# Performance work log

Hardware: AMD Instinct MI355X
Metric: run time of the kernel (lower is better)

Reference implementation:

```python
import jax, jax.numpy as jnp
import numpy as np
from jax.scipy.special import logsumexp

# static problem sizes (all graphs identical size; pairs interleaved [q0,c0,q1,c1,...])
B = 64; NG = 2 * B; N = 48; E = 192; MAX_N = 64; MAX_E = 256
D_IN = 32; D = 128; EDGE_EMB = 128; M = 256; S = 64
T = 5; K = 3; TEMP = 0.1; SINK_ITERS = 10
VN = NG * N; VE = NG * E


def _mlp2(x, W1, b1, W2, b2):
    return jnp.maximum(x @ W1 + b1, 0.0) @ W2 + b2


def setup_inputs():
    keys = iter(jax.random.split(jax.random.key(0), 64))
    def w(fan_in, fan_out):
        return jax.random.normal(next(keys), (fan_in, fan_out), dtype=jnp.float32) * (1.0 / float(np.sqrt(fan_in)))
    z = lambda n: jnp.zeros((n,), jnp.float32)
    inp = {}
    inp['node_features'] = jax.random.normal(next(keys), (VN, D_IN), dtype=jnp.float32)
    inp['edge_features'] = jax.random.normal(next(keys), (VE, D_IN), dtype=jnp.float32)
    off = jnp.repeat(jnp.arange(NG, dtype=jnp.int32) * N, E)
    inp['from_idx'] = jax.random.randint(next(keys), (VE,), 0, N, dtype=jnp.int32) + off
    inp['to_idx'] = jax.random.randint(next(keys), (VE,), 0, N, dtype=jnp.int32) + off
    inp['enc_node_W'] = w(D_IN, D); inp['enc_node_b'] = z(D)
    inp['enc_edge_W'] = w(D_IN, EDGE_EMB); inp['enc_edge_b'] = z(EDGE_EMB)
    inp['ni_W1'] = w(2 * D, 2 * D); inp['ni_b1'] = z(2 * D)
    inp['ni_W2'] = w(2 * D, D); inp['ni_b2'] = z(D)
    ei_in = M + EDGE_EMB
    inp['ei_W1'] = w(ei_in, ei_in); inp['ei_b1'] = z(ei_in)
    inp['ei_W2'] = w(ei_in, EDGE_EMB); inp['ei_b2'] = z(EDGE_EMB)
    inp['msg_W'] = w(2 * D + EDGE_EMB, M); inp['msg_b'] = z(M)
    inp['nu_W1'] = w(D + M, 2 * D); inp['nu_b1'] = z(2 * D)
    inp['nu_W2'] = w(2 * D, D); inp['nu_b2'] = z(D)
    inp['ns_W1'] = w(D, S); inp['ns_b1'] = z(S)
    inp['ns_W2'] = w(S, S); inp['ns_b2'] = z(S)
    inp['es_W1'] = w(M, S); inp['es_b1'] = z(S)
    inp['es_W2'] = w(S, S); inp['es_b2'] = z(S)
    return inp


def _forward(node_features, edge_features, enc_node_W, enc_node_b, enc_edge_W, enc_edge_b,
             ni_W1, ni_b1, ni_W2, ni_b2, ei_W1, ei_b1, ei_W2, ei_b2, msg_W, msg_b,
             nu_W1, nu_b1, nu_W2, nu_b2, ns_W1, ns_b1, ns_W2, ns_b2,
             es_W1, es_b1, es_W2, es_b2, from_idx, to_idx):
    enc_n = node_features @ enc_node_W + enc_node_b            # [VN, D]
    enc_e = edge_features @ enc_edge_W + enc_edge_b            # [VE, EDGE_EMB]
    node_store = jnp.zeros((VN, D * (T + 1)), jnp.float32)
    edge_store = jnp.zeros((VE, M * (T + 1)), jnp.float32)
    # flat index of node/edge j of graph g inside interleaved padded store: g*max + j
    node_pad_idx = (jnp.arange(NG)[:, None] * MAX_N + jnp.arange(N)[None, :]).reshape(-1)
    edge_pad_idx = (jnp.arange(NG)[:, None] * MAX_E + jnp.arange(E)[None, :]).reshape(-1)
    node_mask = (jnp.arange(MAX_N) < N).astype(jnp.float32)[None, :, None]
    edge_mask = (jnp.arange(MAX_E) < E).astype(jnp.float32)[None, :, None]

    def transport(store, n_per, max_set, fdim, sW1, sb1, sW2, sb2, mask):
        x = store.reshape(NG, n_per, store.shape[-1])
        x = jnp.pad(x, ((0, 0), (0, max_set - n_per), (0, 0)))   # pad to max set size
        q, c = x[0::2], x[1::2]                                   # [B, max, dim_total]
        fq, fc = q[:, :, -fdim:], c[:, :, -fdim:]
        tq = _mlp2(fq, sW1, sb1, sW2, sb2) * mask
        tc = _mlp2(fc, sW1, sb1, sW2, sb2) * mask
        la = jnp.einsum('bqs,bcs->bqc', tq, tc) / TEMP
        for _ in range(SINK_ITERS):
            la = la - logsumexp(la, axis=2, keepdims=True)
            la = la - logsumexp(la, axis=1, keepdims=True)
        plan = jnp.exp(la)
        qi = jnp.einsum('bqc,bcd->bqd', plan, c)                  # query <- corpus
        ci = jnp.einsum('bqc,bqd->bcd', plan, q)                  # corpus <- query
        inter = jnp.stack([qi, ci], axis=1).reshape(NG * max_set, -1)
        return plan, inter, fq, fc

    for _ in range(K):  # time_update_steps
        h, e = enc_n, enc_e
        node_slots = [jnp.zeros((VN, D), jnp.float32)]
        edge_slots = [jnp.zeros((VE, M), jnp.float32)]
        for p in range(1, T + 1):  # propagation_steps
            h_comb = _mlp2(jnp.concatenate([h, node_store[:, (p - 1) * D:p * D]], -1), ni_W1, ni_b1, ni_W2, ni_b2)
            e_comb = _mlp2(jnp.concatenate([e, edge_store[:, (p - 1) * M:p * M]], -1), ei_W1, ei_b1, ei_W2, ei_b2)
            src, dst = h_comb[from_idx], h_comb[to_idx]
            fwd_msg = jnp.concatenate([src, dst, e_comb], -1) @ msg_W + msg_b
            bwd_msg = jnp.concatenate([dst, src, e_comb], -1) @ msg_W + msg_b
            agg = jax.ops.segment_sum(fwd_msg, to_idx, num_segments=VN) + jax.ops.segment_sum(bwd_msg, from_idx, num_segments=VN)
            h = _mlp2(jnp.concatenate([h_comb, agg], -1), nu_W1, nu_b1, nu_W2, nu_b2)
            src2, dst2 = h[from_idx], h[to_idx]
            msgs = (jnp.concatenate([src2, dst2, e_comb], -1) @ msg_W + msg_b) + \
                   (jnp.concatenate([dst2, src2, e_comb], -1) @ msg_W + msg_b)
            node_slots.append(h)
            edge_slots.append(msgs)
        upd_node = jnp.concatenate(node_slots, axis=1)
        upd_edge = jnp.concatenate(edge_slots, axis=1)
        n_plan, n_inter, ffq, ffc = transport(upd_node, N, MAX_N, D, ns_W1, ns_b1, ns_W2, ns_b2, node_mask)
        _, e_inter, _, _ = transport(upd_edge, E, MAX_E, M, es_W1, es_b1, es_W2, es_b2, edge_mask)
        node_store = jnp.concatenate([jnp.zeros((VN, D), jnp.float32), n_inter[node_pad_idx, D:]], axis=1)
        edge_store = jnp.concatenate([jnp.zeros((VE, M), jnp.float32), e_inter[edge_pad_idx, M:]], axis=1)

    # feature_alignment_score: -sum relu(q - P c)
    score = -jnp.sum(jnp.maximum(ffq - jnp.einsum('bqc,bcd->bqd', n_plan, ffc), 0.0), axis=(1, 2))
    return score


def reference(node_features, edge_features, from_idx, to_idx, enc_node_W, enc_node_b, enc_edge_W, enc_edge_b,
              ni_W1, ni_b1, ni_W2, ni_b2, ei_W1, ei_b1, ei_W2, ei_b2, msg_W, msg_b,
              nu_W1, nu_b1, nu_W2, nu_b2, ns_W1, ns_b1, ns_W2, ns_b2,
              es_W1, es_b1, es_W2, es_b2):
    return _forward(node_features, edge_features, enc_node_W, enc_node_b, enc_edge_W, enc_edge_b,
                    ni_W1, ni_b1, ni_W2, ni_b2, ei_W1, ei_b1, ei_W2, ei_b2, msg_W, msg_b,
                    nu_W1, nu_b1, nu_W2, nu_b2, ns_W1, ns_b1, ns_W2, ns_b2,
                    es_W1, es_b1, es_W2, es_b2, from_idx, to_idx)
```

## Files before the change

### kernel.cpp

```cpp
#include <hip/hip_runtime.h>
#include <cstdint>
#include <cstddef>

#define NGg   128
#define Bb    64
#define Nn    48
#define Ee    192
#define Sdim  64
#define VNn   6144
#define VEe   24576
#define INV_TEMP 10.0f
#define ADJ_STRIDE 96

typedef unsigned short u16;
typedef unsigned int   u32;
typedef __attribute__((ext_vector_type(8))) short short8;
typedef __attribute__((ext_vector_type(4))) float floatx4;

__device__ __forceinline__ u16 f2bf(float f)
{
    unsigned int u = __float_as_uint(f);
    u += 0x7FFFu + ((u >> 16) & 1u);
    return (u16)(u >> 16);
}
__device__ __forceinline__ float bf2f(u16 h)
{
    return __uint_as_float(((unsigned int)h) << 16);
}

__device__ __forceinline__ u32 packhl(float v)
{
    u16 h = f2bf(v);
    u16 l = f2bf(v - bf2f(h));
    return (u32)h | ((u32)l << 16);
}
__device__ __forceinline__ float unpackhl(u32 w)
{
    return __uint_as_float(w << 16) + __uint_as_float(w & 0xFFFF0000u);
}

#define FL_RELU  1
#define FL_OUTPK 4

#define TW 40

template<int BM, int BN>
__global__ __launch_bounds__(256) void gemm_pk_kernel(
    const u32* __restrict__ A1, int lda1, int K1,
    const u32* __restrict__ A2, int lda2, int K2,
    const u16* __restrict__ Wh, const u16* __restrict__ Wl, int ldwt,
    const float* __restrict__ bias,
    void* __restrict__ Cv, int ldc,
    int Ncap, int flags)
{
    constexpr int FM = BM / 32;
    constexpr int FN = BN / 32;
    constexpr int NA = BM / 8;
    constexpr int NB = BN / 8;
    __shared__ __align__(16) u16 Ah[BM * TW];
    __shared__ __align__(16) u16 Al[BM * TW];
    __shared__ __align__(16) u16 Bh[BN * TW];
    __shared__ __align__(16) u16 Bl[BN * TW];
    const int tid = threadIdx.x;
    const int lane = tid & 63, wave = tid >> 6;
    const int wm = wave >> 1, wn = wave & 1;
// ... 98 lines not shown
                          const u32* A2, int lda2, int K2,
                          const u16* Wh, const u16* Wl, int ldwt,
                          const float* bias,
                          void* C, int ldc, int M, int Ngrid, int Ncap, int flags)
{
    dim3 grid(Ngrid / BN, M / BM);
    if (BM == 128 && BN == 128)
        gemm_pk_kernel<128, 128><<<grid, 256, 0, s>>>(A1, lda1, K1, A2, lda2, K2, Wh, Wl, ldwt, bias, C, ldc, Ncap, flags);
    else if (BM == 128 && BN == 64)
        gemm_pk_kernel<128, 64><<<grid, 256, 0, s>>>(A1, lda1, K1, A2, lda2, K2, Wh, Wl, ldwt, bias, C, ldc, Ncap, flags);
    else if (BM == 64 && BN == 128)
        gemm_pk_kernel<64, 128><<<grid, 256, 0, s>>>(A1, lda1, K1, A2, lda2, K2, Wh, Wl, ldwt, bias, C, ldc, Ncap, flags);
    else
        gemm_pk_kernel<64, 64><<<grid, 256, 0, s>>>(A1, lda1, K1, A2, lda2, K2, Wh, Wl, ldwt, bias, C, ldc, Ncap, flags);
}

struct GemmDesc {
    const u32* A1; int lda1, K1;
    const u32* A2; int lda2, K2;
    const u16* Wh; const u16* Wl; int ldwt;
    const float* bias;
    void* C; int ldc;
    int Ncap, flags, nx, nblk;
};

static inline GemmDesc mkDesc(const u32* A1, int lda1, int K1,
                              const u32* A2, int lda2, int K2,
                              const u16* Wh, const u16* Wl, int ldwt,
                              const float* bias, void* C, int ldc,
                              int M, int Ngrid, int Ncap, int flags)
{
    GemmDesc d;
    d.A1 = A1; d.lda1 = lda1; d.K1 = K1;
    d.A2 = A2; d.lda2 = lda2; d.K2 = K2;
    d.Wh = Wh; d.Wl = Wl; d.ldwt = ldwt;
    d.bias = bias; d.C = C; d.ldc = ldc;
    d.Ncap = Ncap; d.flags = flags;
    d.nx = Ngrid / 128; d.nblk = (M / 128) * (Ngrid / 128);
    return d;
}

__global__ __launch_bounds__(256) void gemm2_pk_kernel(GemmDesc d0, GemmDesc d1, int nb0)
{
    GemmDesc d;
    int local;
    if ((int)blockIdx.x < nb0) { d = d0; local = blockIdx.x; }
    else                       { d = d1; local = blockIdx.x - nb0; }
    const int by = local / d.nx, bx = local % d.nx;
    __shared__ __align__(16) u16 Ah[128 * TW];
    __shared__ __align__(16) u16 Al[128 * TW];
    __shared__ __align__(16) u16 Bh[128 * TW];
    __shared__ __align__(16) u16 Bl[128 * TW];
    const int tid = threadIdx.x;
    const int lane = tid & 63, wave = tid >> 6;
    const int wm = wave >> 1, wn = wave & 1;
    const int bm = by * 128, bn = bx * 128;
    const int K = d.K1 + d.K2;
    const int srow = tid >> 1;
    const int skoff = (tid & 1) * 16;
    const int arow = bm + srow;
    const int brow = bn + srow;
// ... 39 lines not shown
        short8 afh[4], afl[4], bfh[4], bfl[4];
        #pragma unroll
        for (int i = 0; i < 4; i++) {
            const int ro = (wm * 64 + i * 16 + l15) * TW + lq * 8;
            afh[i] = *(const short8*)&Ah[ro];
            afl[i] = *(const short8*)&Al[ro];
        }
        #pragma unroll
        for (int j = 0; j < 4; j++) {
            const int ro = (wn * 64 + j * 16 + l15) * TW + lq * 8;
            bfh[j] = *(const short8*)&Bh[ro];
            bfl[j] = *(const short8*)&Bl[ro];
        }
        #pragma unroll
        for (int i = 0; i < 4; i++)
            #pragma unroll
            for (int j = 0; j < 4; j++) {
                acc[i][j] = __builtin_amdgcn_mfma_f32_16x16x32_bf16(afh[i], bfl[j], acc[i][j], 0, 0, 0);
                acc[i][j] = __builtin_amdgcn_mfma_f32_16x16x32_bf16(afl[i], bfh[j], acc[i][j], 0, 0, 0);
                acc[i][j] = __builtin_amdgcn_mfma_f32_16x16x32_bf16(afh[i], bfh[j], acc[i][j], 0, 0, 0);
            }
        __syncthreads();
    }
    const int relu = d.flags & FL_RELU;
    const int opk  = d.flags & FL_OUTPK;
    #pragma unroll
    for (int j = 0; j < 4; j++) {
        const int col = bn + wn * 64 + j * 16 + l15;
        const bool cok = (col < d.Ncap);
        const float bv = (d.bias && cok) ? d.bias[col] : 0.f;
        #pragma unroll
        for (int i = 0; i < 4; i++) {
            const int row0 = bm + wm * 64 + i * 16 + lq * 4;
            #pragma unroll
            for (int r = 0; r < 4; r++) {
                float v = acc[i][j][r] + bv;
                if (relu) v = fmaxf(v, 0.f);
                if (cok) {
                    if (opk)
                        ((u32*)d.C)[(size_t)(row0 + r) * d.ldc + col] = packhl(v);
                    else
                        ((float*)d.C)[(size_t)(row0 + r) * d.ldc + col] = v;
                }
            }
        }
    }
}

static inline void gemm2(hipStream_t s, const GemmDesc& d0, const GemmDesc& d1)
{
    gemm2_pk_kernel<<<d0.nblk + d1.nblk, 256, 0, s>>>(d0, d1, d0.nblk);
}

__global__ __launch_bounds__(256) void gemm_f32_kernel(
    const float* __restrict__ A, int lda, int K,
    const u16* __restrict__ Wh, const u16* __restrict__ Wl, int ldwt,
    const float* __restrict__ bias, u32* __restrict__ C, int ldc, int Ncap)
{
    __shared__ __align__(16) u16 Ah[128 * TW];
    __shared__ __align__(16) u16 Al[128 * TW];
    __shared__ __align__(16) u16 Bh[128 * TW];
    __shared__ __align__(16) u16 Bl[128 * TW];
    const int tid = threadIdx.x;
    const int lane = tid & 63, wave = tid >> 6;
    const int wm = wave >> 1, wn = wave & 1;
    const int bm = blockIdx.y * 128, bn = blockIdx.x * 128;
    const int srow = tid >> 1;
    const int skoff = (tid & 1) * 16;
    const int arow = bm + srow, brow = bn + srow;
    const int l15 = lane & 15, lq = lane >> 4;

    floatx4 acc[4][4];
    #pragma unroll
    for (int i = 0; i < 4; i++)
// ... 41 lines not shown
        }
        #pragma unroll
        for (int i = 0; i < 4; i++)
            #pragma unroll
            for (int j = 0; j < 4; j++) {
                acc[i][j] = __builtin_amdgcn_mfma_f32_16x16x32_bf16(afh[i], bfl[j], acc[i][j], 0, 0, 0);
                acc[i][j] = __builtin_amdgcn_mfma_f32_16x16x32_bf16(afl[i], bfh[j], acc[i][j], 0, 0, 0);
                acc[i][j] = __builtin_amdgcn_mfma_f32_16x16x32_bf16(afh[i], bfh[j], acc[i][j], 0, 0, 0);
            }
        __syncthreads();
    }
    #pragma unroll
    for (int j = 0; j < 4; j++) {
        const int col = bn + wn * 64 + j * 16 + l15;
        const bool cok = (col < Ncap);
        const float bv = cok ? bias[col] : 0.f;
        #pragma unroll
        for (int i = 0; i < 4; i++) {
            const int row0 = bm + wm * 64 + i * 16 + lq * 4;
            #pragma unroll
            for (int r = 0; r < 4; r++) {
                if (cok)
                    C[(size_t)(row0 + r) * ldc + col] = packhl(acc[i][j][r] + bv);
            }
        }
    }
}

__global__ __launch_bounds__(256) void gemm_ec2msgs_kernel(
    const u32* __restrict__ A,
    const u16* __restrict__ Wh, const u16* __restrict__ Wl, int ldwt,
    const float* __restrict__ bias,
    const float* __restrict__ Qs,
    const int* __restrict__ from_idx, const int* __restrict__ to_idx,
    u32* __restrict__ M)
{
    __shared__ __align__(16) u16 Ah[128 * TW];
    __shared__ __align__(16) u16 Al[128 * TW];
    __shared__ __align__(16) u16 Bh[128 * TW];
    __shared__ __align__(16) u16 Bl[128 * TW];
    const int tid = threadIdx.x;
    const int lane = tid & 63, wave = tid >> 6;
    const int wm = wave >> 1, wn = wave & 1;
    const int bm = blockIdx.y * 128, bn = blockIdx.x * 128;
    const int srow = tid >> 1;
    const int skoff = (tid & 1) * 16;

    floatx4 acc[4][4];
    #pragma unroll
    for (int i = 0; i < 4; i++)
        #pragma unroll
        for (int j = 0; j < 4; j++) acc[i][j] = (floatx4){0.f, 0.f, 0.f, 0.f};

    const int arow = bm + srow;
    const int brow = bn + srow;
    const int l15 = lane & 15, lq = lane >> 4;

    for (int k0 = 0; k0 < 128; k0 += 32) {
        const int kk = k0 + skoff;
        const u32* asrc = A + (size_t)arow * 128 + kk;
        u32 pk[16];
        ((uint4*)pk)[0] = ((const uint4*)asrc)[0];
        ((uint4*)pk)[1] = ((const uint4*)asrc)[1];
        ((uint4*)pk)[2] = ((const uint4*)asrc)[2];
        ((uint4*)pk)[3] = ((const uint4*)asrc)[3];
        u32 hi8[8], lo8[8];
        #pragma unroll
        for (int q = 0; q < 8; q++) {
            hi8[q] = __builtin_amdgcn_perm(pk[2 * q + 1], pk[2 * q], 0x05040100u);
            lo8[q] = __builtin_amdgcn_perm(pk[2 * q + 1], pk[2 * q], 0x07060302u);
        }
        *(uint4*)&Ah[srow * TW + skoff]     = ((uint4*)hi8)[0];
        *(uint4*)&Ah[srow * TW + skoff + 8] = ((uint4*)hi8)[1];
        *(uint4*)&Al[srow * TW + skoff]     = ((uint4*)lo8)[0];
        *(uint4*)&Al[srow * TW + skoff + 8] = ((uint4*)lo8)[1];
        const u16* bh = Wh + (size_t)brow * ldwt + kk;
        const u16* bl = Wl + (size_t)brow * ldwt + kk;
        *(uint4*)&Bh[srow * TW + skoff]     = ((const uint4*)bh)[0];
        *(uint4*)&Bh[srow * TW + skoff + 8] = ((const uint4*)bh)[1];
        *(uint4*)&Bl[srow * TW + skoff]     = ((const uint4*)bl)[0];
        *(uint4*)&Bl[srow * TW + skoff + 8] = ((const uint4*)bl)[1];
        __syncthreads();
        short8 afh[4], afl[4], bfh[4], bfl[4];
        #pragma unroll
        for (int i = 0; i < 4; i++) {
            const int ro = (wm * 64 + i * 16 + l15) * TW + lq * 8;
            afh[i] = *(const short8*)&Ah[ro];
            afl[i] = *(const short8*)&Al[ro];
        }
        #pragma unroll
        for (int j = 0; j < 4; j++) {
            const int ro = (wn * 64 + j * 16 + l15) * TW + lq * 8;
            bfh[j] = *(const short8*)&Bh[ro];
            bfl[j] = *(const short8*)&Bl[ro];
        }
        #pragma unroll
        for (int i = 0; i < 4; i++)
            #pragma unroll
            for (int j = 0; j < 4; j++) {
                acc[i][j] = __builtin_amdgcn_mfma_f32_16x16x32_bf16(afh[i], bfl[j], acc[i][j], 0, 0, 0);
                acc[i][j] = __builtin_amdgcn_mfma_f32_16x16x32_bf16(afl[i], bfh[j], acc[i][j], 0, 0, 0);
                acc[i][j] = __builtin_amdgcn_mfma_f32_16x16x32_bf16(afh[i], bfh[j], acc[i][j], 0, 0, 0);
            }
        __syncthreads();
    }
    #pragma unroll
    for (int i = 0; i < 4; i++) {
        #pragma unroll
        for (int r = 0; r < 4; r++) {
            const int row = bm + wm * 64 + i * 16 + lq * 4 + r;
            const int fi = from_idx[row], ti = to_idx[row];
            #pragma unroll
            for (int j = 0; j < 4; j++) {
                const int col = bn + wn * 64 + j * 16 + l15;
                float v = 2.f * (acc[i][j][r] + bias[col])
                        + Qs[(size_t)fi * 256 + col] + Qs[(size_t)ti * 256 + col];
                M[(size_t)row * 256 + col] = packhl(v);
            }
        }
    }
}

__global__ __launch_bounds__(256) void prep_kernel(
    const float* __restrict__ niW1, const float* __restrict__ niW2,
    const float* __restrict__ eiW1, const float* __restrict__ eiW2,
    const float* __restrict__ msgW, const float* __restrict__ nuW1,
    const float* __restrict__ nuW2, const float* __restrict__ encnW,
    const float* __restrict__ enceW, const float* __restrict__ nsW1,
    const float* __restrict__ nsW2, const float* __restrict__ esW1,
    const float* __restrict__ esW2,
    u16* __restrict__ WT, u16* __restrict__ WTL)
{
    int idx = blockIdx.x * 256 + threadIdx.x;
    if (idx >= 696320) return;
    const float* src; int base, N, Npad, ldk, noff = 0, wtoff;
    int wsum = 0;
    if      (idx < 65536)  { src = niW1;  base = 0;      N = 256; Npad = 256; ldk = 256; wtoff = 0; }
    else if (idx < 98304)  { src = niW2;  base = 65536;  N = 128; Npad = 128; ldk = 256; wtoff = 65536; }
    else if (idx < 245760) { src = eiW1;  base = 98304;  N = 384; Npad = 384; ldk = 384; wtoff = 98304; }
    else if (idx < 294912) { src = eiW2;  base = 245760; N = 128; Npad = 128; ldk = 384; wtoff = 245760; }
// ... 3 lines not shown
    else if (idx < 557056) { src = nuW1;  base = 458752; N = 256; Npad = 256; ldk = 384; wtoff = 458752; }
    else if (idx < 589824) { src = nuW2;  base = 557056; N = 128; Npad = 128; ldk = 256; wtoff = 557056; }
    else if (idx < 622592) { src = msgW;  base = 589824; N = 256; Npad = 256; ldk = 128; wtoff = 589824; wsum = 1; }
    else if (idx < 626688) { src = encnW; base = 622592; N = 128; Npad = 128; ldk = 32;  wtoff = 622592; }
    else if (idx < 630784) { src = enceW; base = 626688; N = 128; Npad = 128; ldk = 32;  wtoff = 626688; }
    else if (idx < 647168) { src = nsW1;  base = 630784; N = 64;  Npad = 128; ldk = 128; wtoff = 630784; }
    else if (idx < 655360) { src = nsW2;  base = 647168; N = 64;  Npad = 128; ldk = 64;  wtoff = 647168; }
    else if (idx < 688128) { src = esW1;  base = 655360; N = 64;  Npad = 128; ldk = 256; wtoff = 655360; }
    else                   { src = esW2;  base = 688128; N = 64;  Npad = 128; ldk = 64;  wtoff = 688128; }
    int rel = idx - base;
    int k = rel / Npad, n = rel % Npad;
    float v = 0.f;
    if (n < N) {
        v = src[(size_t)k * N + n];
        if (wsum) v += src[32768 + (size_t)k * N + n];
    }
    u16 h = f2bf(v);
    size_t o = (size_t)wtoff + (size_t)(noff + n) * ldk + k;
    WT[o] = h;
    WTL[o] = f2bf(v - bf2f(h));
}

__global__ __launch_bounds__(256) void bgemm_dual_kernel(
    const float* __restrict__ P, int ms, int n_per,
    const u32* __restrict__ U, int ldu,
    u32* __restrict__ C, int ldc, int nxh)
{
    __shared__ __align__(16) u16 Ah[64 * TW];
    __shared__ __align__(16) u16 Al[64 * TW];
    __shared__ __align__(16) u16 Bh[128 * TW];
    __shared__ __align__(16) u16 Bl[128 * TW];
    const int b = blockIdx.z;
    const float* Pb = P + (size_t)b * ms * ms;
    const int bxr = blockIdx.x;
    const int transp = (bxr >= nxh) ? 1 : 0;
    const int bn = (bxr - transp * nxh) * 128;
    const int qbase = (2 * b) * n_per, cbase = (2 * b + 1) * n_per;
    const int obase = transp ? cbase : qbase;
    const int ibase = transp ? qbase : cbase;
    const int bm = blockIdx.y * 64;
    const int tid = threadIdx.x, lane = tid & 63, wave = tid >> 6;
    const int wm = wave >> 1, wn = wave & 1;
    const int l15 = lane & 15, lq = lane >> 4;
    const int sar = tid >> 2, sak = (tid & 3) * 8;
    const int sbn = tid >> 1, sbk = (tid & 1) * 16;
    const int Kpad = (n_per + 31) & ~31;

    floatx4 acc[2][4];
    #pragma unroll
    for (int i = 0; i < 2; i++)
        #pragma unroll
        for (int j = 0; j < 4; j++) acc[i][j] = (floatx4){0.f, 0.f, 0.f, 0.f};

    for (int k0 = 0; k0 < Kpad; k0 += 32) {
        {
            u16 ph[8], pl8[8];
            const int m = bm + sar;
            #pragma unroll
            for (int i = 0; i < 8; i++) {
                int kk = k0 + sak + i;
                float v = 0.f;
                if (kk < n_per && m < n_per)
                    v = transp ? Pb[(size_t)kk * ms + m] : Pb[(size_t)m * ms + kk];
                u16 h = f2bf(v);
                ph[i] = h; pl8[i] = f2bf(v - bf2f(h));
            }
            *(uint4*)&Ah[sar * TW + sak] = *(const uint4*)&ph[0];
            *(uint4*)&Al[sar * TW + sak] = *(const uint4*)&pl8[0];
        }
        {
            u16 qh[16], ql[16];
            #pragma unroll
            for (int i = 0; i < 16; i++) {
                int kk = k0 + sbk + i;
                u32 w = 0;
                if (kk < n_per) w = U[(size_t)(ibase + kk) * ldu + bn + sbn];
                qh[i] = (u16)w; ql[i] = (u16)(w >> 16);
            }
            *(uint4*)&Bh[sbn * TW + sbk]     = *(const uint4*)&qh[0];
            *(uint4*)&Bh[sbn * TW + sbk + 8] = *(const uint4*)&qh[8];
            *(uint4*)&Bl[sbn * TW + sbk]     = *(const uint4*)&ql[0];
            *(uint4*)&Bl[sbn * TW + sbk + 8] = *(const uint4*)&ql[8];
        }
        __syncthreads();
        short8 afh[2], afl[2], bfh[4], bfl[4];
        #pragma unroll
        for (int i = 0; i < 2; i++) {
            const int ro = (wm * 32 + i * 16 + l15) * TW + lq * 8;
            afh[i] = *(const short8*)&Ah[ro];
            afl[i] = *(const short8*)&Al[ro];
        }
// ... 9 lines not shown
            for (int j = 0; j < 4; j++) {
                acc[i][j] = __builtin_amdgcn_mfma_f32_16x16x32_bf16(afh[i], bfl[j], acc[i][j], 0, 0, 0);
                acc[i][j] = __builtin_amdgcn_mfma_f32_16x16x32_bf16(afl[i], bfh[j], acc[i][j], 0, 0, 0);
                acc[i][j] = __builtin_amdgcn_mfma_f32_16x16x32_bf16(afh[i], bfh[j], acc[i][j], 0, 0, 0);
            }
        __syncthreads();
    }
    #pragma unroll
    for (int j = 0; j < 4; j++) {
        const int col = bn + wn * 64 + j * 16 + l15;
        #pragma unroll
        for (int i = 0; i < 2; i++) {
            const int row0 = bm + wm * 32 + i * 16 + lq * 4;
            #pragma unroll
            for (int r = 0; r < 4; r++) {
                const int m = row0 + r;
                if (m < n_per)
                    C[(size_t)(obase + m) * ldc + col] = packhl(acc[i][j][r]);
            }
        }
    }
}

static inline void bgemmDual(hipStream_t s, const float* P, int ms, int n_per,
                             const u32* U, int ldu, u32* C, int ldc, int N)
{
    int nxh = N / 128;
    dim3 grid(nxh * 2, (n_per + 63) / 64, Bb);
    bgemm_dual_kernel<<<grid, 256, 0, s>>>(P, ms, n_per, U, ldu, C, ldc, nxh);
}

__global__ __launch_bounds__(256) void la_sinkhorn64_kernel(
    const float* __restrict__ tt, float* __restrict__ n_la)
{
    const int b = blockIdx.x;
    __shared__ float Aq[64][65];
    __shared__ float Ac[64][65];
    __shared__ float m[64][65];
    __shared__ float v_s[64];
    __shared__ float part[4][64];
    const int tid = threadIdx.x;
    const int lane = tid & 63, w = tid >> 6;
    for (int idx = tid; idx < 4096; idx += 256) {
        int r = idx >> 6, s = idx & 63;
        float vq = 0.f, vc = 0.f;
        if (r < Nn) {
            vq = tt[((size_t)(2 * b) * Nn + r) * Sdim + s];
            vc = tt[((size_t)(2 * b + 1) * Nn + r) * Sdim + s];
        }
        Aq[r][s] = vq;
        Ac[r][s] = vc;
    }
    __syncthreads();
    {
        const int tx = tid & 15, ty = tid >> 4;
        float acc[4][4] = {};
// ... 28 lines not shown
        u[j] = mx;
    }
    for (int it = 0; it < 10; it++) {
        float vr = v_s[lane];
        #pragma unroll
        for (int j = 0; j < 16; j++) {
            float s = __expf(x[j] - vr - u[j]);
            #pragma unroll
            for (int d = 1; d < 64; d <<= 1) s += __shfl_xor(s, d);
            u[j] += __logf(s);
        }
        float s = 0.f;
        #pragma unroll
        for (int j = 0; j < 16; j++) s += __expf(x[j] - u[j] - vr);
        part[w][lane] = s;
        __syncthreads();
        if (tid < 64) {
            float ss = part[0][tid] + part[1][tid] + part[2][tid] + part[3][tid];
            v_s[tid] += __logf(ss);
        }
        __syncthreads();
    }
    float vr = v_s[lane];
    float* g = n_la + (size_t)b * 4096;
    #pragma unroll
    for (int j = 0; j < 16; j++)
        g[(size_t)(w * 16 + j) * 64 + lane] = __expf(x[j] - u[j] - vr);
}

__global__ __launch_bounds__(256) void la_gemm256_kernel(
    const float* __restrict__ tt, float* __restrict__ la)
{
    const int b = blockIdx.z;
    const int bm = blockIdx.y * 64, bn = blockIdx.x * 64;
    __shared__ float Aq[64][65];
    __shared__ float Ac[64][65];
    const int tid = threadIdx.x;
    for (int idx = tid; idx < 4096; idx += 256) {
        int r = idx >> 6, s = idx & 63;
        float vq = 0.f, vc = 0.f;
        int qr = bm + r, cr = bn + r;
        if (qr < Ee) vq = tt[((size_t)(2 * b) * Ee + qr) * Sdim + s];
        if (cr < Ee) vc = tt[((size_t)(2 * b + 1) * Ee + cr) * Sdim + s];
        Aq[r][s] = vq;
        Ac[r][s] = vc;
    }
    __syncthreads();
    const int tx = tid & 15, ty = tid >> 4;
    float acc[4][4] = {};
    for (int s = 0; s < 64; s++) {
// ... 50 lines not shown
            #pragma unroll
            for (int d = 1; d < 64; d <<= 1) s += __shfl_xor(s, d);
            u[j] += __logf(s);
            const float inv = 1.f / s;
            cp0 = fmaf(e0, inv, cp0);
            cp1 = fmaf(e1, inv, cp1);
            cp2 = fmaf(e2, inv, cp2);
            cp3 = fmaf(e3, inv, cp3);
        }
        *(float4*)&part[w][lane][0] = (float4){cp0, cp1, cp2, cp3};
        __syncthreads();
        if (tid < 256) {
            const int cl = tid >> 2, cq = tid & 3;
            float ss = 0.f;
            #pragma unroll
            for (int w2 = 0; w2 < 16; w2++) ss += part[w2][cl][cq];
            v_s[tid] += __logf(ss);
        }
        __syncthreads();
    }
    const float4 vr = *(const float4*)&v_s[4 * lane];
    #pragma unroll
    for (int j = 0; j < 16; j++) {
        float4 o;
        o.x = __expf(x[j].x - u[j] - vr.x);
        o.y = __expf(x[j].y - u[j] - vr.y);
        o.z = __expf(x[j].z - u[j] - vr.z);
        o.w = __expf(x[j].w - u[j] - vr.w);
        ((float4*)(g + (size_t)(w * 16 + j) * 256))[lane] = o;
    }
}

__global__ __launch_bounds__(256) void zero_deg_kernel(int* __restrict__ deg)
{
    deg[blockIdx.x * 256 + threadIdx.x] = 0;
}

__global__ __launch_bounds__(256) void csr_build_kernel(
    const int* __restrict__ from_idx, const int* __restrict__ to_idx,
    int* __restrict__ deg, u32* __restrict__ adj)
{
    int e = blockIdx.x * 256 + threadIdx.x;
    if (e >= VEe) return;
    int f = from_idx[e], t = to_idx[e];
    int p1 = atomicAdd(&deg[t], 1);
    if (p1 < ADJ_STRIDE) adj[(size_t)t * ADJ_STRIDE + p1] = ((u32)e << 13) | (u32)f;
    int p2 = atomicAdd(&deg[f], 1);
    if (p2 < ADJ_STRIDE) adj[(size_t)f * ADJ_STRIDE + p2] = ((u32)e << 13) | (u32)t;
}

__global__ __launch_bounds__(256) void agg_csr_kernel(
    const u32* __restrict__ P01,
// ... 16 lines not shown
        a += unpackhl(ec2[(size_t)e * 256 + d]) + unpackhl(P01[(size_t)pr * 512 + d]);
    }
    agg[(size_t)n * 256 + d] = packhl(a);
}

__global__ __launch_bounds__(256) void msgs_inplace_kernel(
    u32* __restrict__ m, const float* __restrict__ Qs,
    const int* __restrict__ from_idx, const int* __restrict__ to_idx)
{
    const int e = blockIdx.x;
    const int d = threadIdx.x;
    const int f = from_idx[e], t = to_idx[e];
    size_t o = (size_t)e * 256 + d;
    float v = Qs[(size_t)f * 256 + d] + Qs[(size_t)t * 256 + d] + 2.f * unpackhl(m[o]);
    m[o] = packhl(v);
}

__global__ void diag_kernel(float* __restrict__ out, float v)
{
    out[threadIdx.x] = v;
}

__global__ __launch_bounds__(128) void score_kernel(
    const u32* __restrict__ upd_node, const float* __restrict__ plan,
    float* __restrict__ out)
{
    const int b = blockIdx.x;
    const int tid = threadIdx.x;
    __shared__ float ffc[48][128];
    __shared__ float pl[64][48];
    __shared__ float red[128];
    for (int c = 0; c < 48; c++)
        ffc[c][tid] = unpackhl(upd_node[(size_t)((2 * b + 1) * 48 + c) * 640 + 512 + tid]);
    for (int idx = tid; idx < 64 * 48; idx += 128) {
        int q = idx / 48, c = idx % 48;
        pl[q][c] = plan[(size_t)b * 4096 + q * 64 + c];
    }
    __syncthreads();
    float accv = 0.f;
    for (int q = 0; q < 64; q++) {
        float rsum = 0.f;
        #pragma unroll 8
        for (int c = 0; c < 48; c++) rsum = fmaf(pl[q][c], ffc[c][tid], rsum);
        float fq = 0.f;
        if (q < 48) fq = unpackhl(upd_node[(size_t)((2 * b) * 48 + q) * 640 + 512 + tid]);
        accv += fmaxf(fq - rsum, 0.f);
    }
    red[tid] = accv;
    __syncthreads();
    for (int sft = 64; sft > 0; sft >>= 1) {
        if (tid < sft) red[tid] += red[tid + sft];
        __syncthreads();
    }
    if (tid == 0) out[b] = -red[0];
}

#define OFF_UPD_NODE   0ULL
#define OFF_NODE_STORE 3932160ULL
#define OFF_EDGE_STORE 7077888ULL
// ... 68 lines not shown
    const float* es_b2 = (const float*)d_in[29];

    float* ws = (float*)d_ws;
    float* upd_node   = ws + OFF_UPD_NODE;
    float* node_store = ws + OFF_NODE_STORE;
    float* edge_store = ws + OFF_EDGE_STORE;
    float* ecomb      = ws + OFF_ECOMB;
    float* enc_n      = ws + OFF_ENC_N;
    float* enc_e      = ws + OFF_ENC_E;
    float* n_la       = ws + OFF_N_LA;
    u16* WT  = (u16*)(ws + OFF_WT);
    u16* WTL = (u16*)(ws + OFF_WTL);
    float* arena      = ws + OFF_ARENA;
    int* deg = (int*)(ws + OFF_DEG);
    u32* adj = (u32*)(ws + OFF_ADJ);

    float* A_hidden = arena;
    float* A_hcomb  = arena + 1572864;
    float* A_ehid   = arena + 2359296;
    float* A_ec2    = arena + 2359296;
    float* A_P01    = arena + 8650752;
    float* A_aggb   = arena + 11796480;
    float* B_Qs       = arena;
    float* B_thid_e   = arena + 8650752;
    float* B_ttreal_e = arena + 10223616;
    float* B_ela      = arena + 2359296;
    float* B_msgs     = arena + 6553600;
    float* B_thid_n   = arena + 12058624;
    float* B_ttreal_n = arena + 12451840;

    prep_kernel<<<(696320 + 255) / 256, 256, 0, stream>>>(
        ni_W1, ni_W2, ei_W1, ei_W2, msg_W, nu_W1, nu_W2,
        enc_node_W, enc_edge_W, ns_W1, ns_W2, es_W1, es_W2, WT, WTL);
    zero_deg_kernel<<<VNn / 256, 256, 0, stream>>>(deg);
    csr_build_kernel<<<VEe / 256, 256, 0, stream>>>(from_idx, to_idx, deg, adj);

    gemm_f32_kernel<<<dim3(1, VNn / 128), 256, 0, stream>>>(
        node_features, 32, 32, WT + WT_ENCN, WTL + WT_ENCN, 32, enc_node_b, PK(enc_n), 128, 128);
    gemm_f32_kernel<<<dim3(1, VEe / 128), 256, 0, stream>>>(
        edge_features, 32, 32, WT + WT_ENCE, WTL + WT_ENCE, 32, enc_edge_b, PK(enc_e), 128, 128);

    for (int k = 0; k < 3; k++) {
        for (int p = 1; p <= 5; p++) {
            const bool hs = (k > 0) && (p > 1);
            const u32* hA1 = (p == 1) ? PK(enc_n) : PK(upd_node + (size_t)(p - 2) * 128);
            const int  hlda1 = (p == 1) ? 128 : 640;
// ... 36 lines not shown
                       ni_b2, A_hcomb, 128, VNn, 128, 128, FL_OUTPK);
                gemmPK(stream, 64, 128, PK(A_hcomb), 128, 128, nullptr, 0, 0,
                       WT + WT_P01, WTL + WT_P01, 128,
                       nullptr, A_P01, 512, VNn, 512, 512, FL_OUTPK);
            } else {
                gemmPK(stream, 64, 128, hA1, hlda1, 128, hA2, 512, hK2,
                       WT + WT_NIW1, WTL + WT_NIW1, 256, ni_b1,
                       A_hidden, 256, VNn, 256, 256, FL_RELU | FL_OUTPK);
                gemmPK(stream, 64, 64, PK(A_hidden), 256, 256, nullptr, 0, 0,
                       WT + WT_NIW2, WTL + WT_NIW2, 256,
                       ni_b2, A_hcomb, 128, VNn, 128, 128, FL_OUTPK);
                gemmPK(stream, 64, 128, PK(A_hcomb), 128, 128, nullptr, 0, 0,
                       WT + WT_P01, WTL + WT_P01, 128,
                       nullptr, A_P01, 512, VNn, 512, 512, FL_OUTPK);
            }
            agg_csr_kernel<<<VNn, 256, 0, stream>>>(PK(A_P01), PK(A_ec2), deg, adj, PK(A_aggb));
            gemmPK(stream, 64, 128, PK(A_hcomb), 128, 128, PK(A_aggb), 256, 256,
                   WT + WT_NUW1, WTL + WT_NUW1, 384,
                   nu_b1, A_hidden, 256, VNn, 256, 256, FL_RELU | FL_OUTPK);
            gemmPK(stream, 64, 64, PK(A_hidden), 256, 256, nullptr, 0, 0,
                   WT + WT_NUW2, WTL + WT_NUW2, 256,
                   nu_b2, upd_node + (size_t)(p - 1) * 128, 640, VNn, 128, 128, FL_OUTPK);
        }
        gemmPK(stream, 64, 64, PK(upd_node + 512), 640, 128, nullptr, 0, 0,
               WT + WT_NS1, WTL + WT_NS1, 128,
               ns_b1, B_thid_n, 64, VNn, 64, 64, FL_RELU | FL_OUTPK);
        gemmPK(stream, 64, 64, PK(B_thid_n), 64, 64, nullptr, 0, 0,
               WT + WT_NS2, WTL + WT_NS2, 64,
               ns_b2, B_ttreal_n, 64, VNn, 64, 64, 0);
        la_sinkhorn64_kernel<<<Bb, 256, 0, stream>>>(B_ttreal_n, n_la);
        if (k < 2) {
            bgemmDual(stream, n_la, 64, 48, PK(upd_node), 640, PK(node_store), 512, 512);
            gemmPK(stream, 64, 128, PK(upd_node + 512), 640, 128, nullptr, 0, 0,
                   WT + WT_WSUM, WTL + WT_WSUM, 128,
                   nullptr, B_Qs, 256, VNn, 256, 256, 0);
            msgs_inplace_kernel<<<VEe, 256, 0, stream>>>(PK(A_ec2), B_Qs, from_idx, to_idx);
            gemmPK(stream, 128, 64, PK(A_ec2), 256, 256, nullptr, 0, 0,
                   WT + WT_ES1, WTL + WT_ES1, 256,
                   es_b1, B_thid_e, 64, VEe, 64, 64, FL_RELU | FL_OUTPK);
            gemmPK(stream, 128, 64, PK(B_thid_e), 64, 64, nullptr, 0, 0,
                   WT + WT_ES2, WTL + WT_ES2, 64,
                   es_b2, B_ttreal_e, 64, VEe, 64, 64, 0);
            la_gemm256_kernel<<<dim3(4, 4, Bb), 256, 0, stream>>>(B_ttreal_e, B_ela);
            sinkhorn256_kernel<<<Bb, 1024, 0, stream>>>(B_ela);
            for (int sl = 1; sl <= 4; sl++) {
                const size_t ss = (k == 0) ? 0 : (size_t)(sl - 1);
                gemmPK(stream, 64, 128, PK(upd_node + (size_t)(sl - 1) * 128), 640, 128,
                       nullptr, 0, 0,
                       WT + WT_WSUM, WTL + WT_WSUM, 128,
                       nullptr, B_Qs, 256, VNn, 256, 256, 0);
                gemm_ec2msgs_kernel<<<dim3(2, VEe / 128), 256, 0, stream>>>(
                    PK(ecomb + ss * VEe * 128),
                    WT + WT_MSG + 256, WTL + WT_MSG + 256, 384,
                    msg_b, B_Qs, from_idx, to_idx, PK(B_msgs));
                bgemmDual(stream, B_ela, 256, 192, PK(B_msgs), 256,
                          PK(edge_store + (size_t)(sl - 1) * 256), 1024, 256);
            }
        }
    }
    score_kernel<<<Bb, 128, 0, stream>>>(PK(upd_node), n_la, (float*)d_out);
}
```

Before: 3.147 ms.

## Batch node/edge scoring GEMMs into dual launches and pipeline Qs with message GEMM

The node and edge scoring MLP GEMMs are merged pairwise into single dual-descriptor launches. The message GEMM now runs as a mode of the generic dual GEMM kernel, and the next slice's Qs GEMM is computed in the same launch using double-buffered Qs storage. Sinkhorn plans are stored pre-split as packed hi/lo bf16, so the batched plan GEMM loads them directly instead of converting from fp32. The aim is fewer kernel launches, better GPU fill from co-scheduled small GEMMs, and less conversion work, at the cost of a second Qs buffer placed in ecomb memory and more scheduling complexity.

```diff
diff --git a/kernel.cpp b/kernel.cpp
--- a/kernel.cpp
+++ b/kernel.cpp
@@ -41,6 +41,7 @@
 
 #define FL_RELU  1
 #define FL_OUTPK 4
+#define FL_MSGS  8
 
 #define TW 40
 
@@ -185,6 +186,8 @@
     const float* bias;
     void* C; int ldc;
     int Ncap, flags, nx, nblk;
+    const float* qs;
+    const int* fidx; const int* tidx;
 };
 
 static inline GemmDesc mkDesc(const u32* A1, int lda1, int K1,
@@ -200,6 +203,7 @@
     d.bias = bias; d.C = C; d.ldc = ldc;
     d.Ncap = Ncap; d.flags = flags;
     d.nx = Ngrid / 128; d.nblk = (M / 128) * (Ngrid / 128);
+    d.qs = nullptr; d.fidx = nullptr; d.tidx = nullptr;
     return d;
 }
 
@@ -285,6 +289,24 @@
             }
         __syncthreads();
     }
+    if (d.flags & FL_MSGS) {
+        #pragma unroll
+        for (int i = 0; i < 4; i++) {
+            #pragma unroll
+            for (int r = 0; r < 4; r++) {
+                const int row = bm + wm * 64 + i * 16 + lq * 4 + r;
+                const int fi = d.fidx[row], ti = d.tidx[row];
+                #pragma unroll
+                for (int j = 0; j < 4; j++) {
+                    const int col = bn + wn * 64 + j * 16 + l15;
+                    float v = 2.f * (acc[i][j][r] + d.bias[col])
+                            + d.qs[(size_t)fi * 256 + col] + d.qs[(size_t)ti * 256 + col];
+                    ((u32*)d.C)[(size_t)row * d.ldc + col] = packhl(v);
+                }
+            }
+        }
+        return;
+    }
     const int relu = d.flags & FL_RELU;
     const int opk  = d.flags & FL_OUTPK;
     #pragma unroll
@@ -313,6 +335,10 @@
 static inline void gemm2(hipStream_t s, const GemmDesc& d0, const GemmDesc& d1)
 {
     gemm2_pk_kernel<<<d0.nblk + d1.nblk, 256, 0, s>>>(d0, d1, d0.nblk);
+}
+static inline void gemm1(hipStream_t s, const GemmDesc& d0)
+{
+    gemm2_pk_kernel<<<d0.nblk, 256, 0, s>>>(d0, d0, d0.nblk);
 }
 
 __global__ __launch_bounds__(256) void gemm_f32_kernel(
@@ -400,100 +426,6 @@
             for (int r = 0; r < 4; r++) {
                 if (cok)
                     C[(size_t)(row0 + r) * ldc + col] = packhl(acc[i][j][r] + bv);
-            }
-        }
-    }
-}
-
-__global__ __launch_bounds__(256) void gemm_ec2msgs_kernel(
-    const u32* __restrict__ A,
-    const u16* __restrict__ Wh, const u16* __restrict__ Wl, int ldwt,
-    const float* __restrict__ bias,
-    const float* __restrict__ Qs,
-    const int* __restrict__ from_idx, const int* __restrict__ to_idx,
-    u32* __restrict__ M)
-{
-    __shared__ __align__(16) u16 Ah[128 * TW];
-    __shared__ __align__(16) u16 Al[128 * TW];
-    __shared__ __align__(16) u16 Bh[128 * TW];
-    __shared__ __align__(16) u16 Bl[128 * TW];
-    const int tid = threadIdx.x;
-    const int lane = tid & 63, wave = tid >> 6;
-    const int wm = wave >> 1, wn = wave & 1;
-    const int bm = blockIdx.y * 128, bn = blockIdx.x * 128;
-    const int srow = tid >> 1;
-    const int skoff = (tid & 1) * 16;
-
-    floatx4 acc[4][4];
-    #pragma unroll
-    for (int i = 0; i < 4; i++)
-        #pragma unroll
-        for (int j = 0; j < 4; j++) acc[i][j] = (floatx4){0.f, 0.f, 0.f, 0.f};
-
-    const int arow = bm + srow;
-    const int brow = bn + srow;
-    const int l15 = lane & 15, lq = lane >> 4;
-
-    for (int k0 = 0; k0 < 128; k0 += 32) {
-        const int kk = k0 + skoff;
-        const u32* asrc = A + (size_t)arow * 128 + kk;
-        u32 pk[16];
-        ((uint4*)pk)[0] = ((const uint4*)asrc)[0];
-        ((uint4*)pk)[1] = ((const uint4*)asrc)[1];
-        ((uint4*)pk)[2] = ((const uint4*)asrc)[2];
-        ((uint4*)pk)[3] = ((const uint4*)asrc)[3];
-        u32 hi8[8], lo8[8];
-        #pragma unroll
-        for (int q = 0; q < 8; q++) {
-            hi8[q] = __builtin_amdgcn_perm(pk[2 * q + 1], pk[2 * q], 0x05040100u);
-            lo8[q] = __builtin_amdgcn_perm(pk[2 * q + 1], pk[2 * q], 0x07060302u);
-        }
-        *(uint4*)&Ah[srow * TW + skoff]     = ((uint4*)hi8)[0];
-        *(uint4*)&Ah[srow * TW + skoff + 8] = ((uint4*)hi8)[1];
-        *(uint4*)&Al[srow * TW + skoff]     = ((uint4*)lo8)[0];
-        *(uint4*)&Al[srow * TW + skoff + 8] = ((uint4*)lo8)[1];
-        const u16* bh = Wh + (size_t)brow * ldwt + kk;
-        const u16* bl = Wl + (size_t)brow * ldwt + kk;
-        *(uint4*)&Bh[srow * TW + skoff]     = ((const uint4*)bh)[0];
-        *(uint4*)&Bh[srow * TW + skoff + 8] = ((const uint4*)bh)[1];
-        *(uint4*)&Bl[srow * TW + skoff]     = ((const uint4*)bl)[0];
-        *(uint4*)&Bl[srow * TW + skoff + 8] = ((const uint4*)bl)[1];
-        __syncthreads();
-        short8 afh[4], afl[4], bfh[4], bfl[4];
-        #pragma unroll
-        for (int i = 0; i < 4; i++) {
-            const int ro = (wm * 64 + i * 16 + l15) * TW + lq * 8;
-            afh[i] = *(const short8*)&Ah[ro];
-            afl[i] = *(const short8*)&Al[ro];
-        }
-        #pragma unroll
-        for (int j = 0; j < 4; j++) {
-            const int ro = (wn * 64 + j * 16 + l15) * TW + lq * 8;
-            bfh[j] = *(const short8*)&Bh[ro];
-            bfl[j] = *(const short8*)&Bl[ro];
-        }
-        #pragma unroll
-        for (int i = 0; i < 4; i++)
-            #pragma unroll
-            for (int j = 0; j < 4; j++) {
-                acc[i][j] = __builtin_amdgcn_mfma_f32_16x16x32_bf16(afh[i], bfl[j], acc[i][j], 0, 0, 0);
-                acc[i][j] = __builtin_amdgcn_mfma_f32_16x16x32_bf16(afl[i], bfh[j], acc[i][j], 0, 0, 0);
-                acc[i][j] = __builtin_amdgcn_mfma_f32_16x16x32_bf16(afh[i], bfh[j], acc[i][j], 0, 0, 0);
-            }
-        __syncthreads();
-    }
-    #pragma unroll
-    for (int i = 0; i < 4; i++) {
-        #pragma unroll
-        for (int r = 0; r < 4; r++) {
-            const int row = bm + wm * 64 + i * 16 + lq * 4 + r;
-            const int fi = from_idx[row], ti = to_idx[row];
-            #pragma unroll
-            for (int j = 0; j < 4; j++) {
-                const int col = bn + wn * 64 + j * 16 + l15;
-                float v = 2.f * (acc[i][j][r] + bias[col])
-                        + Qs[(size_t)fi * 256 + col] + Qs[(size_t)ti * 256 + col];
-                M[(size_t)row * 256 + col] = packhl(v);
             }
         }
     }
@@ -543,7 +475,7 @@
 }
 
 __global__ __launch_bounds__(256) void bgemm_dual_kernel(
-    const float* __restrict__ P, int ms, int n_per,
+    const u32* __restrict__ P, int ms, int n_per,
     const u32* __restrict__ U, int ldu,
     u32* __restrict__ C, int ldc, int nxh)
 {
@@ -552,7 +484,7 @@
     __shared__ __align__(16) u16 Bh[128 * TW];
     __shared__ __align__(16) u16 Bl[128 * TW];
     const int b = blockIdx.z;
-    const float* Pb = P + (size_t)b * ms * ms;
+    const u32* Pb = P + (size_t)b * ms * ms;
     const int bxr = blockIdx.x;
     const int transp = (bxr >= nxh) ? 1 : 0;
     const int bn = (bxr - transp * nxh) * 128;
@@ -575,19 +507,33 @@
 
     for (int k0 = 0; k0 < Kpad; k0 += 32) {
         {
-            u16 ph[8], pl8[8];
             const int m = bm + sar;
-            #pragma unroll
-            for (int i = 0; i < 8; i++) {
-                int kk = k0 + sak + i;
-                float v = 0.f;
-                if (kk < n_per && m < n_per)
-                    v = transp ? Pb[(size_t)kk * ms + m] : Pb[(size_t)m * ms + kk];
-                u16 h = f2bf(v);
-                ph[i] = h; pl8[i] = f2bf(v - bf2f(h));
-            }
-            *(uint4*)&Ah[sar * TW + sak] = *(const uint4*)&ph[0];
-            *(uint4*)&Al[sar * TW + sak] = *(const uint4*)&pl8[0];
+            u32 pk[8];
+            if (m < n_per) {
+                if (!transp) {
+                    const u32* src = Pb + (size_t)m * ms + k0 + sak;
+                    ((uint4*)pk)[0] = ((const uint4*)src)[0];
+                    ((uint4*)pk)[1] = ((const uint4*)src)[1];
+                } else {
+                    #pragma unroll
+                    for (int i = 0; i < 8; i++)
+                        pk[i] = Pb[(size_t)(k0 + sak + i) * ms + m];
+                }
+                #pragma unroll
+                for (int i = 0; i < 8; i++)
+                    if (k0 + sak + i >= n_per) pk[i] = 0;
+            } else {
+                #pragma unroll
+                for (int i = 0; i < 8; i++) pk[i] = 0;
+            }
+            u32 hi[4], lo[4];
+            #pragma unroll
+            for (int q = 0; q < 4; q++) {
+                hi[q] = __builtin_amdgcn_perm(pk[2 * q + 1], pk[2 * q], 0x05040100u);
+                lo[q] = __builtin_amdgcn_perm(pk[2 * q + 1], pk[2 * q], 0x07060302u);
+            }
+            *(uint4*)&Ah[sar * TW + sak] = *(uint4*)hi;
+            *(uint4*)&Al[sar * TW + sak] = *(uint4*)lo;
         }
         {
             u16 qh[16], ql[16];
@@ -643,7 +589,7 @@
     }
 }
 
-static inline void bgemmDual(hipStream_t s, const float* P, int ms, int n_per,
+static inline void bgemmDual(hipStream_t s, const u32* P, int ms, int n_per,
                              const u32* U, int ldu, u32* C, int ldc, int N)
 {
     int nxh = N / 128;
@@ -652,7 +598,7 @@
 }
 
 __global__ __launch_bounds__(256) void la_sinkhorn64_kernel(
-    const float* __restrict__ tt, float* __restrict__ n_la)
+    const float* __restrict__ tt, u32* __restrict__ n_la)
 {
     const int b = blockIdx.x;
     __shared__ float Aq[64][65];
@@ -727,10 +673,10 @@
         __syncthreads();
     }
     float vr = v_s[lane];
-    float* g = n_la + (size_t)b * 4096;
+    u32* g = n_la + (size_t)b * 4096;
     #pragma unroll
     for (int j = 0; j < 16; j++)
-        g[(size_t)(w * 16 + j) * 64 + lane] = __expf(x[j] - u[j] - vr);
+        g[(size_t)(w * 16 + j) * 64 + lane] = packhl(__expf(x[j] - u[j] - vr));
 }
 
 __global__ __launch_bounds__(256) void la_gemm256_kernel(
@@ -827,12 +773,12 @@
     const float4 vr = *(const float4*)&v_s[4 * lane];
     #pragma unroll
     for (int j = 0; j < 16; j++) {
-        float4 o;
-        o.x = __expf(x[j].x - u[j] - vr.x);
-        o.y = __expf(x[j].y - u[j] - vr.y);
-        o.z = __expf(x[j].z - u[j] - vr.z);
-        o.w = __expf(x[j].w - u[j] - vr.w);
-        ((float4*)(g + (size_t)(w * 16 + j) * 256))[lane] = o;
+        u32 o[4];
+        o[0] = packhl(__expf(x[j].x - u[j] - vr.x));
+        o[1] = packhl(__expf(x[j].y - u[j] - vr.y));
+        o[2] = packhl(__expf(x[j].z - u[j] - vr.z));
+        o[3] = packhl(__expf(x[j].w - u[j] - vr.w));
+        ((uint4*)(g + (size_t)(w * 16 + j) * 256))[lane] = *(uint4*)o;
     }
 }
 
@@ -895,7 +841,7 @@
 }
 
 __global__ __launch_bounds__(128) void score_kernel(
-    const u32* __restrict__ upd_node, const float* __restrict__ plan,
+    const u32* __restrict__ upd_node, const u32* __restrict__ plan,
     float* __restrict__ out)
 {
     const int b = blockIdx.x;
@@ -907,7 +853,7 @@
         ffc[c][tid] = unpackhl(upd_node[(size_t)((2 * b + 1) * 48 + c) * 640 + 512 + tid]);
     for (int idx = tid; idx < 64 * 48; idx += 128) {
         int q = idx / 48, c = idx % 48;
-        pl[q][c] = plan[(size_t)b * 4096 + q * 64 + c];
+        pl[q][c] = unpackhl(plan[(size_t)b * 4096 + q * 64 + c]);
     }
     __syncthreads();
     float accv = 0.f;
@@ -1022,6 +968,7 @@
     float* A_P01    = arena + 8650752;
     float* A_aggb   = arena + 11796480;
     float* B_Qs       = arena;
+    float* B_Qs2      = ecomb + (size_t)4 * VEe * 128;
     float* B_thid_e   = arena + 8650752;
     float* B_ttreal_e = arena + 10223616;
     float* B_ela      = arena + 2359296;
@@ -1104,41 +1051,62 @@
                    WT + WT_NUW2, WTL + WT_NUW2, 256,
                    nu_b2, upd_node + (size_t)(p - 1) * 128, 640, VNn, 128, 128, FL_OUTPK);
         }
-        gemmPK(stream, 64, 64, PK(upd_node + 512), 640, 128, nullptr, 0, 0,
-               WT + WT_NS1, WTL + WT_NS1, 128,
-               ns_b1, B_thid_n, 64, VNn, 64, 64, FL_RELU | FL_OUTPK);
-        gemmPK(stream, 64, 64, PK(B_thid_n), 64, 64, nullptr, 0, 0,
-               WT + WT_NS2, WTL + WT_NS2, 64,
-               ns_b2, B_ttreal_n, 64, VNn, 64, 64, 0);
-        la_sinkhorn64_kernel<<<Bb, 256, 0, stream>>>(B_ttreal_n, n_la);
         if (k < 2) {
-            bgemmDual(stream, n_la, 64, 48, PK(upd_node), 640, PK(node_store), 512, 512);
             gemmPK(stream, 64, 128, PK(upd_node + 512), 640, 128, nullptr, 0, 0,
                    WT + WT_WSUM, WTL + WT_WSUM, 128,
                    nullptr, B_Qs, 256, VNn, 256, 256, 0);
             msgs_inplace_kernel<<<VEe, 256, 0, stream>>>(PK(A_ec2), B_Qs, from_idx, to_idx);
-            gemmPK(stream, 128, 64, PK(A_ec2), 256, 256, nullptr, 0, 0,
-                   WT + WT_ES1, WTL + WT_ES1, 256,
-                   es_b1, B_thid_e, 64, VEe, 64, 64, FL_RELU | FL_OUTPK);
-            gemmPK(stream, 128, 64, PK(B_thid_e), 64, 64, nullptr, 0, 0,
-                   WT + WT_ES2, WTL + WT_ES2, 64,
-                   es_b2, B_ttreal_e, 64, VEe, 64, 64, 0);
+            GemmDesc es1_d = mkDesc(PK(A_ec2), 256, 256, nullptr, 0, 0,
+                                    WT + WT_ES1, WTL + WT_ES1, 256, es_b1,
+                                    B_thid_e, 64, VEe, 128, 64, FL_RELU | FL_OUTPK);
+            GemmDesc ns1_d = mkDesc(PK(upd_node + 512), 640, 128, nullptr, 0, 0,
+                                    WT + WT_NS1, WTL + WT_NS1, 128, ns_b1,
+                                    B_thid_n, 64, VNn, 128, 64, FL_RELU | FL_OUTPK);
+            gemm2(stream, es1_d, ns1_d);
+            GemmDesc es2_d = mkDesc(PK(B_thid_e), 64, 64, nullptr, 0, 0,
+                                    WT + WT_ES2, WTL + WT_ES2, 64, es_b2,
+                                    B_ttreal_e, 64, VEe, 128, 64, 0);
+            GemmDesc ns2_d = mkDesc(PK(B_thid_n), 64, 64, nullptr, 0, 0,
+                                    WT + WT_NS2, WTL + WT_NS2, 64, ns_b2,
+                                    B_ttreal_n, 64, VNn, 128, 64, 0);
+            gemm2(stream, es2_d, ns2_d);
+            la_sinkhorn64_kernel<<<Bb, 256, 0, stream>>>(B_ttreal_n, PK(n_la));
             la_gemm256_kernel<<<dim3(4, 4, Bb), 256, 0, stream>>>(B_ttreal_e, B_ela);
             sinkhorn256_kernel<<<Bb, 1024, 0, stream>>>(B_ela);
+            bgemmDual(stream, PK(n_la), 64, 48, PK(upd_node), 640, PK(node_store), 512, 512);
+            float* qsbuf[2] = { B_Qs2, B_Qs };
+            GemmDesc qs1_d = mkDesc(PK(upd_node), 640, 128, nullptr, 0, 0,
+                                    WT + WT_WSUM, WTL + WT_WSUM, 128, nullptr,
+                                    qsbuf[0], 256, VNn, 256, 256, 0);
+            gemm1(stream, qs1_d);
             for (int sl = 1; sl <= 4; sl++) {
                 const size_t ss = (k == 0) ? 0 : (size_t)(sl - 1);
-                gemmPK(stream, 64, 128, PK(upd_node + (size_t)(sl - 1) * 128), 640, 128,
-                       nullptr, 0, 0,
-                       WT + WT_WSUM, WTL + WT_WSUM, 128,
-                       nullptr, B_Qs, 256, VNn, 256, 256, 0);
-                gemm_ec2msgs_kernel<<<dim3(2, VEe / 128), 256, 0, stream>>>(
-                    PK(ecomb + ss * VEe * 128),
-                    WT + WT_MSG + 256, WTL + WT_MSG + 256, 384,
-                    msg_b, B_Qs, from_idx, to_idx, PK(B_msgs));
-                bgemmDual(stream, B_ela, 256, 192, PK(B_msgs), 256,
+                GemmDesc em_d = mkDesc(PK(ecomb + ss * VEe * 128), 128, 128, nullptr, 0, 0,
+                                       WT + WT_MSG + 256, WTL + WT_MSG + 256, 384, msg_b,
+                                       B_msgs, 256, VEe, 256, 256, FL_MSGS);
+                em_d.qs = qsbuf[(sl - 1) & 1];
+                em_d.fidx = from_idx; em_d.tidx = to_idx;
+                if (sl < 4) {
+                    GemmDesc qsn_d = mkDesc(PK(upd_node + (size_t)sl * 128), 640, 128,
+                                            nullptr, 0, 0,
+                                            WT + WT_WSUM, WTL + WT_WSUM, 128, nullptr,
+                                            qsbuf[sl & 1], 256, VNn, 256, 256, 0);
+                    gemm2(stream, em_d, qsn_d);
+                } else {
+                    gemm1(stream, em_d);
+                }
+                bgemmDual(stream, PK(B_ela), 256, 192, PK(B_msgs), 256,
                           PK(edge_store + (size_t)(sl - 1) * 256), 1024, 256);
             }
-        }
-    }
-    score_kernel<<<Bb, 128, 0, stream>>>(PK(upd_node), n_la, (float*)d_out);
-}
+        } else {
+            gemmPK(stream, 64, 64, PK(upd_node + 512), 640, 128, nullptr, 0, 0,
+                   WT + WT_NS1, WTL + WT_NS1, 128,
+                   ns_b1, B_thid_n, 64, VNn, 64, 64, FL_RELU | FL_OUTPK);
+            gemmPK(stream, 64, 64, PK(B_thid_n), 64, 64, nullptr, 0, 0,
+                   WT + WT_NS2, WTL + WT_NS2, 64,
+                   ns_b2, B_ttreal_n, 64, VNn, 64, 64, 0);
+            la_sinkhorn64_kernel<<<Bb, 256, 0, stream>>>(B_ttreal_n, PK(n_la));
+        }
+    }
+    score_kernel<<<Bb, 128, 0, stream>>>(PK(upd_node), PK(n_la), (float*)d_out);
+}
```

Result: faster. 2.916 ms (-7.3%).
